# Kernel tuning notes

Measured on AMD Instinct MI355X. Metric: run time of the kernel, lower is better.

Reference implementation:

```python
import jax, jax.numpy as jnp
import numpy as np

H = 768    # bert hidden size
P = 64     # num dialogue pairs
L = 2 * P  # interleaved (user,system) sequence length
C = 2      # num_classes (CRF tags)
LAM = 0.1  # lambda_mle


def setup_inputs():
    key = jax.random.key(0)
    ks = jax.random.split(key, 21)
    def rn(k, shape, s=0.05):
        return jax.random.normal(k, shape, dtype=jnp.float32) * s
    G = 4 * H
    return {
        "user_repr": rn(ks[0], (P, H), 1.0),
        "system_repr": rn(ks[1], (P, H), 1.0),
        "post_Wih0": rn(ks[2], (2, G, H)), "post_Whh0": rn(ks[3], (2, G, H)), "post_b0": rn(ks[4], (2, G)),
        "post_Wih1": rn(ks[5], (2, G, 2 * H)), "post_Whh1": rn(ks[6], (2, G, H)), "post_b1": rn(ks[7], (2, G)),
        "prior_Wih0": rn(ks[8], (2, G, H)), "prior_Whh0": rn(ks[9], (2, G, H)), "prior_b0": rn(ks[10], (2, G)),
        "prior_Wih1": rn(ks[11], (2, G, 2 * H)), "prior_Whh1": rn(ks[12], (2, G, H)), "prior_b1": rn(ks[13], (2, G)),
        "post_proj_W": rn(ks[14], (C, 2 * H)), "post_proj_b": rn(ks[15], (C,)),
        "prior_proj_W": rn(ks[16], (C, 2 * H)), "prior_proj_b": rn(ks[17], (C,)),
        "transitions": rn(ks[18], (C, C), 0.1),
        "user_I_label": jax.random.randint(ks[19], (1, P), 0, C),
        "system_I_label": jax.random.randint(ks[20], (1, P), 0, C),
    }


def _lstm_dir(x, mask, Wih, Whh, b, reverse):
    # x: [P, L, Din]; mask: [P, L] bool (True = valid step). Masked steps freeze state,
    # so each row computes the LSTM over its own prefix exactly as the per-pair loop does.
    Pn, Ln, _ = x.shape
    Hn = Whh.shape[1]
    xw = jnp.einsum('pld,gd->plg', x, Wih) + b  # [P, L, 4H] input projections (torch gate order i,f,g,o)
    def step(carry, inp):
        h, c = carry
        xw_t, m_t = inp
        gates = xw_t + h @ Whh.T
        i, f, g, o = jnp.split(gates, 4, axis=-1)
        c2 = jax.nn.sigmoid(f) * c + jax.nn.sigmoid(i) * jnp.tanh(g)
        h2 = jax.nn.sigmoid(o) * jnp.tanh(c2)
        m = m_t[:, None]
        h = jnp.where(m, h2, h)
        c = jnp.where(m, c2, c)
        return (h, c), h
    init = (jnp.zeros((Pn, Hn), x.dtype), jnp.zeros((Pn, Hn), x.dtype))
    _, hs = jax.lax.scan(step, init, (jnp.swapaxes(xw, 0, 1), mask.T), reverse=reverse)
    return jnp.swapaxes(hs, 0, 1)  # [P, L, H]


def _bilstm(x, mask, layers):
    for Wih, Whh, b in layers:
        fwd = _lstm_dir(x, mask, Wih[0], Whh[0], b[0], False)
        bwd = _lstm_dir(x, mask, Wih[1], Whh[1], b[1], True)
        x = jnp.concatenate([fwd, bwd], axis=-1)
    return x


def _forward(user_repr, system_repr,
             post_Wih0, post_Whh0, post_b0, post_Wih1, post_Whh1, post_b1,
             prior_Wih0, prior_Whh0, prior_b0, prior_Wih1, prior_Whh1, prior_b1,
             post_proj_W, post_proj_b, prior_proj_W, prior_proj_b, transitions, labs):
    seq = jnp.stack([user_repr, system_repr], axis=1).reshape(L, H)  # interleaved u0,s0,u1,s1,...
    l = 2 * (jnp.arange(P) + 1)                 # prefix length per pair
    t = jnp.arange(L)
    mask = t[None, :] < l[:, None]              # [P, L]
    xb = jnp.broadcast_to(seq[None], (P, L, H))
    # posterior branch: biLSTM over each prefix, then emissions
    post_out = _bilstm(xb, mask, [(post_Wih0, post_Whh0, post_b0), (post_Wih1, post_Whh1, post_b1)])
    em = post_out @ post_proj_W.T + post_proj_b  # [P, L, C]
    mf = mask.astype(em.dtype)
    # CRF gold score per pair
    e_lab = jnp.take_along_axis(em, jnp.broadcast_to(labs[None, :, None], (P, L, 1)), axis=2)[..., 0]
    trans_step = transitions[labs[:-1], labs[1:]]  # [L-1]
    gold = (e_lab * mf).sum(1) + (trans_step[None, :] * mf[:, 1:]).sum(1)
    # CRF forward algorithm (log partition), masked scan over time
    def fstep(alpha, inp):
        em_t, m_t = inp  # [P, C], [P]
        new = jax.nn.logsumexp(alpha[:, :, None] + transitions[None, :, :] + em_t[:, None, :], axis=1)
        return jnp.where(m_t[:, None], new, alpha), None
    alpha, _ = jax.lax.scan(fstep, em[:, 0, :], (jnp.swapaxes(em[:, 1:, :], 0, 1), mask[:, 1:].T))
    total = jax.nn.logsumexp(alpha, axis=1)
    loss_crf = jnp.mean(total - gold)
    # prior branch: prefix minus last token, take last valid hidden
    mask_p = t[None, :] < (l - 1)[:, None]
    prior_out = _bilstm(xb, mask_p, [(prior_Wih0, prior_Whh0, prior_b0), (prior_Wih1, prior_Whh1, prior_b1)])
    prior_last = jnp.take_along_axis(prior_out, jnp.broadcast_to((l - 2)[:, None, None], (P, 1, 2 * H)), axis=1)[:, 0, :]
    prior_emis = prior_last @ prior_proj_W.T + prior_proj_b  # [P, C]
    post_last = jnp.take_along_axis(em, jnp.broadcast_to((l - 1)[:, None, None], (P, 1, C)), axis=1)[:, 0, :]
    loss_mle = jnp.mean((prior_emis - jax.lax.stop_gradient(post_last)) ** 2)
    return loss_crf, loss_mle, loss_crf + LAM * loss_mle


def reference(user_repr, system_repr,
              post_Wih0, post_Whh0, post_b0, post_Wih1, post_Whh1, post_b1,
              prior_Wih0, prior_Whh0, prior_b0, prior_Wih1, prior_Whh1, prior_b1,
              post_proj_W, post_proj_b, prior_proj_W, prior_proj_b, transitions,
              user_I_label, system_I_label):
    labs = jnp.stack([user_I_label[0], system_I_label[0]], axis=1).reshape(L)
    return _forward(user_repr, system_repr,
                    post_Wih0, post_Whh0, post_b0, post_Wih1, post_Whh1, post_b1,
                    prior_Wih0, prior_Whh0, prior_b0, prior_Wih1, prior_Whh1, prior_b1,
                    post_proj_W, post_proj_b, prior_proj_W, prior_proj_b, transitions, labs)
```

## Files before the change

kernel.cpp:

```cpp
#include <hip/hip_runtime.h>


typedef short v8s __attribute__((ext_vector_type(8)));
typedef float v4f __attribute__((ext_vector_type(4)));
typedef unsigned short u16;

#define MFMA(a, b, c) __builtin_amdgcn_mfma_f32_16x16x32_bf16((a), (b), (c), 0, 0, 0)

static constexpr size_t WMAT    = (size_t)96 * 3072 * 8;
static constexpr size_t SLOT64  = (size_t)96 * 64 * 8;
static constexpr size_t SLOT16  = (size_t)96 * 16 * 8;
static constexpr size_t SLOT128 = (size_t)96 * 128 * 8;

static constexpr size_t OFF_CALL = 0;
static constexpr size_t SZ_CALL  = (size_t)8 * 64 * 768 * 4;
static constexpr size_t OFF_EM   = OFF_CALL + SZ_CALL;
static constexpr size_t SZ_EM    = (size_t)2 * 64 * 128 * 2 * 4;
static constexpr size_t OFF_XW0  = OFF_EM + SZ_EM;
static constexpr size_t SZ_XW    = (size_t)4 * 128 * 3072 * 4;
static constexpr size_t OFF_XW1  = OFF_XW0 + SZ_XW;
static constexpr size_t OFF_SEQ  = OFF_XW1 + SZ_XW;
static constexpr size_t SZ_SEQ   = (size_t)96 * 128 * 8 * 2;
static constexpr size_t OFF_LABS = OFF_SEQ + SZ_SEQ;
static constexpr size_t SZ_LABS  = 512;
static constexpr size_t OFF_W0   = OFF_LABS + SZ_LABS;
static constexpr size_t SZ_W4    = (size_t)4 * WMAT * 2;
static constexpr size_t OFF_W1X  = OFF_W0 + SZ_W4;
static constexpr size_t OFF_W1R  = OFF_W1X + SZ_W4;
static constexpr size_t OFF_F0   = OFF_W1R + SZ_W4;
static constexpr size_t SZ_F0    = (size_t)2 * 129 * SLOT16 * 2;
static constexpr size_t OFF_H0F  = OFF_F0 + SZ_F0;
static constexpr size_t SZ_H0F   = (size_t)2 * SLOT128 * 2;
static constexpr size_t OFF_B0   = OFF_H0F + SZ_H0F;
static constexpr size_t SZ_S64   = (size_t)2 * 129 * SLOT64 * 2;
static constexpr size_t OFF_F1   = OFF_B0 + SZ_S64;
static constexpr size_t OFF_B1   = OFF_F1 + SZ_S64;
static constexpr size_t WS_NEED  = OFF_B1 + SZ_S64;

static __device__ __forceinline__ u16 f2b(float f) {
  unsigned int u = __float_as_uint(f);
  unsigned int r = (u + 0x7FFFu + ((u >> 16) & 1u)) >> 16;
  return (u16)r;
}
static __device__ __forceinline__ float b2f(u16 u) {
  return __uint_as_float(((unsigned int)u) << 16);
}
static __device__ __forceinline__ float sigf(float x) {
  return 1.0f / (1.0f + __expf(-x));
}
static __device__ __forceinline__ float tanhfast(float x) {
  return 1.0f - 2.0f / (__expf(2.0f * x) + 1.0f);
}
static __device__ __forceinline__ float lse2(float a, float b) {
  float mx = fmaxf(a, b);
  return mx + __logf(__expf(a - mx) + __expf(b - mx));
}

static __device__ __forceinline__ void stage_w(const u16* mat, int kb0, int jb, u16* lds) {
  const int4* src = (const int4*)mat;
  int4* dst = (int4*)lds;
  int tid = threadIdx.x;
#pragma unroll
  for (int it = 0; it < 12; ++it) {
    int ck = it * 256 + tid;
    int kb = ck >> 6;
    int r = ck & 63;
    int g = (r >> 4) * 768 + jb + (r & 15);
    dst[ck] = src[(size_t)(kb0 + kb) * 3072 + g];
  }
}

__global__ void init_zero(float* c_all, u16* f0a, u16* f0b, u16* b0a, u16* b0b,
                          u16* f1a, u16* f1b, u16* b1a, u16* b1b) {
  int idx = blockIdx.x * 256 + threadIdx.x;
  c_all[idx] = 0.0f;
  if (idx < (int)SLOT16) { f0a[idx] = 0; f0b[idx] = 0; }
  if (idx < (int)SLOT64) {
    b0a[idx] = 0; b0b[idx] = 0;
    f1a[idx] = 0; f1b[idx] = 0;
    b1a[idx] = 0; b1b[idx] = 0;
  }
}

__global__ void build_seq(const float* user, const float* sysr, const int* ulab,
                          const int* slab, u16* seqkp, int* labs) {
  int idx = blockIdx.x * 256 + threadIdx.x;
  int t = idx / 768;
  int hh = idx - t * 768;
  float v = (t & 1) ? sysr[(t >> 1) * 768 + hh] : user[(t >> 1) * 768 + hh];
  seqkp[((size_t)(hh >> 3) * 128 + t) * 8 + (hh & 7)] = f2b(v);
  if (idx < 128) labs[idx] = (idx & 1) ? slab[idx >> 1] : ulab[idx >> 1];
}

__global__ void cvt_w(const float* postWhh0, const float* priWhh0,
                      const float* postWih1, const float* priWih1,
                      const float* postWhh1, const float* priWhh1,
                      u16* W0kp, u16* W1xkp, u16* W1rkp) {
  int mat = blockIdx.y;
  int grp = mat >> 2;
  int sub = mat & 3;
  int m = sub >> 1;
  int dirw = sub & 1;
  const float* src;
  int stride, coff;
  u16* dstb;
  if (grp == 0)      { src = m ? priWhh0 : postWhh0; stride = 768;  coff = 0;   dstb = W0kp; }
  else if (grp == 1) { src = m ? priWih1 : postWih1; stride = 1536; coff = 768; dstb = W1xkp; }
  else               { src = m ? priWhh1 : postWhh1; stride = 768;  coff = 0;   dstb = W1rkp; }
  src += (size_t)dirw * 3072 * stride;
  int cid = blockIdx.x * 256 + threadIdx.x;
  int g = cid / 96;
  int kb = cid - g * 96;
  const float* s = src + (size_t)g * stride + coff + (size_t)kb * 8;
  union { u16 h[8]; int4 v; } u;
#pragma unroll
  for (int j = 0; j < 8; ++j) u.h[j] = f2b(s[j]);
  ((int4*)(dstb + (size_t)sub * WMAT))[(size_t)kb * 3072 + g] = u.v;
}

__global__ void __launch_bounds__(256) xw_gemm(const u16* Akp, unsigned long long Astride,
                                               const float* Wm0, const float* Wm1, int wstride,
                                               const float* bm0, const float* bm1, float* out) {
  __shared__ u16 lds[48 * 64 * 8];
  int tid = threadIdx.x;
  int lane = tid & 63;
  int wave = tid >> 6;
  int md = blockIdx.y;
  int m = md >> 1;
  int dir = md & 1;
  const u16* A = Akp + (size_t)m * Astride;
  const float* W = (m ? Wm1 : Wm0) + (size_t)dir * 3072 * wstride;
  const float* b = (m ? bm1 : bm0) + dir * 3072;
  int g0 = blockIdx.x * 64;
  int quad = lane >> 4, l15 = lane & 15;
  v4f acc[2][4];
#pragma unroll
  for (int a = 0; a < 2; ++a)
#pragma unroll
    for (int nt = 0; nt < 4; ++nt) acc[a][nt] = (v4f){0.f, 0.f, 0.f, 0.f};

  for (int hfl = 0; hfl < 2; ++hfl) {
    if (hfl) __syncthreads();
    for (int it = 0; it < 12; ++it) {
      int ck = it * 256 + tid;
      int kb = ck >> 6;
      int r = ck & 63;
      int g = g0 + r;
      const float* s = W + (size_t)g * wstride + (size_t)(hfl * 48 + kb) * 8;
      union { u16 h[8]; int4 v; } u;
#pragma unroll
      for (int j = 0; j < 8; ++j) u.h[j] = f2b(s[j]);
      *(int4*)(lds + (size_t)ck * 8) = u.v;
    }
    __syncthreads();
    for (int lt = 0; lt < 12; ++lt) {
      int kblk = (hfl * 12 + lt) * 4 + quad;
      v8s a0 = ((const v8s*)A)[(size_t)kblk * 128 + (wave * 2 + 0) * 16 + l15];
      v8s a1 = ((const v8s*)A)[(size_t)kblk * 128 + (wave * 2 + 1) * 16 + l15];
#pragma unroll
      for (int nt = 0; nt < 4; ++nt) {
        v8s bb = *(const v8s*)(lds + ((size_t)((lt * 4 + quad) * 64) + nt * 16 + l15) * 8);
        acc[0][nt] = MFMA(a0, bb, acc[0][nt]);
        acc[1][nt] = MFMA(a1, bb, acc[1][nt]);
      }
    }
  }
#pragma unroll
  for (int a = 0; a < 2; ++a)
#pragma unroll
    for (int nt = 0; nt < 4; ++nt) {
      int g = g0 + nt * 16 + l15;
      float bv = b[g];
#pragma unroll
      for (int r = 0; r < 4; ++r) {
        int trow = (wave * 2 + a) * 16 + quad * 4 + r;
        out[(size_t)(md * 128 + trow) * 3072 + g] = acc[a][nt][r] + bv;
      }
    }
}

__global__ void __launch_bounds__(256) stepA_k(int t, const u16* W0kp, const float* xw0,
                                               u16* B0, u16* F0, u16* h0f, float* c_all) {
  __shared__ u16 lds[48 * 64 * 8];
  int tid = threadIdx.x;
  int lane = tid & 63;
  int wave = tid >> 6;
  int c = blockIdx.y;
  int isf = c >> 1;
  int m = c & 1;
  int dir = isf ? 0 : 1;
  int jb = blockIdx.x * 16;
  int quad = lane >> 4, l15 = lane & 15;
  const u16* mat = W0kp + (size_t)(m * 2 + dir) * WMAT;
  const u16* Asrc;
  int R, rowbase;
  if (isf) { Asrc = F0 + (size_t)(m * 129 + t) * SLOT16; R = 16; rowbase = 0; }
  else     { Asrc = B0 + (size_t)(m * 129 + t + 1) * SLOT64; R = 64; rowbase = wave * 16; }
  v4f acc[4];
#pragma unroll
  for (int gt = 0; gt < 4; ++gt) acc[gt] = (v4f){0.f, 0.f, 0.f, 0.f};
  bool docomp = (!isf) || (wave == 0);

  for (int hfl = 0; hfl < 2; ++hfl) {
    if (hfl) __syncthreads();
    stage_w(mat, hfl * 48, jb, lds);
    __syncthreads();
    if (docomp) {
      for (int lt = 0; lt < 12; ++lt) {
        int kblk = hfl * 48 + lt * 4 + quad;
        v8s a = ((const v8s*)Asrc)[(size_t)kblk * R + rowbase + l15];
#pragma unroll
        for (int gt = 0; gt < 4; ++gt) {
          v8s bb = *(const v8s*)(lds + ((size_t)((lt * 4 + quad) * 4 + gt) * 16 + l15) * 8);
          acc[gt] = MFMA(a, bb, acc[gt]);
        }
      }
    }
  }
  if (!docomp) return;

  int j = jb + l15;
  const float* xw = xw0 + (size_t)((m * 2 + dir) * 128 + t) * 3072;
  float xi = xw[j], xf = xw[768 + j], xg = xw[1536 + j], xo = xw[2304 + j];
  float* cs = c_all + (size_t)c * 64 * 768;
  if (!isf) {
    u16* dst = B0 + (size_t)(m * 129 + t) * SLOT64;
#pragma unroll
    for (int r = 0; r < 4; ++r) {
      int p = wave * 16 + quad * 4 + r;
      float gi = sigf(acc[0][r] + xi), gf = sigf(acc[1][r] + xf);
      float gg = tanhfast(acc[2][r] + xg), go = sigf(acc[3][r] + xo);
      float cold = cs[(size_t)p * 768 + j];
      float cn = gf * cold + gi * gg;
      float hn = go * tanhfast(cn);
      int lenp = 2 * p + 2 - m;
      bool act = t < lenp;
      float ce = act ? cn : 0.f;
      float he = act ? hn : 0.f;
      cs[(size_t)p * 768 + j] = ce;
      dst[((size_t)(j >> 3) * 64 + p) * 8 + (j & 7)] = f2b(he);
    }
  } else {
    if (quad == 0) {
      float gi = sigf(acc[0][0] + xi), gf = sigf(acc[1][0] + xf);
      float gg = tanhfast(acc[2][0] + xg), go = sigf(acc[3][0] + xo);
      float cold = cs[j];
      float cn = gf * cold + gi * gg;
      float hn = go * tanhfast(cn);
      cs[j] = cn;
      F0[(size_t)(m * 129 + t + 1) * SLOT16 + ((size_t)(j >> 3) * 16) * 8 + (j & 7)] = f2b(hn);
      h0f[(size_t)m * SLOT128 + ((size_t)(j >> 3) * 128 + t) * 8 + (j & 7)] = f2b(hn);
    }
  }
}

__global__ void __launch_bounds__(256) stepB_k(int t, const u16* W1x, const u16* W1r,
                                               const float* xw1s, const u16* B0, u16* F1,
                                               u16* B1, float* c_all) {
  __shared__ u16 lds[48 * 64 * 8];
  int tid = threadIdx.x;
  int lane = tid & 63;
  int wave = tid >> 6;
  int md = blockIdx.y;
  int m = md >> 1;
  int dir = md & 1;
  int jb = blockIdx.x * 16;
  int quad = lane >> 4, l15 = lane & 15;
  const u16* A1 = B0 + (size_t)(m * 129 + t) * SLOT64;
  const u16* A2 = dir ? (const u16*)(B1 + (size_t)(m * 129 + t + 1) * SLOT64)
                      : (const u16*)(F1 + (size_t)(m * 129 + t) * SLOT64);
  v4f acc[4];
#pragma unroll
  for (int gt = 0; gt < 4; ++gt) acc[gt] = (v4f){0.f, 0.f, 0.f, 0.f};

  for (int q = 0; q < 4; ++q) {
    if (q) __syncthreads();
    const u16* mat = (q < 2 ? W1x : W1r) + (size_t)md * WMAT;
    stage_w(mat, (q & 1) * 48, jb, lds);
    __syncthreads();
    const u16* As = (q < 2) ? A1 : A2;
    int akb0 = (q & 1) * 48;
    for (int lt = 0; lt < 12; ++lt) {
      v8s a = ((const v8s*)As)[(size_t)(akb0 + lt * 4 + quad) * 64 + wave * 16 + l15];
#pragma unroll
      for (int gt = 0; gt < 4; ++gt) {
        v8s bb = *(const v8s*)(lds + ((size_t)((lt * 4 + quad) * 4 + gt) * 16 + l15) * 8);
        acc[gt] = MFMA(a, bb, acc[gt]);
      }
    }
  }

  int j = jb + l15;
  const float* xw = xw1s + (size_t)(md * 128 + t) * 3072;
  float xi = xw[j], xf = xw[768 + j], xg = xw[1536 + j], xo = xw[2304 + j];
  float* cs = c_all + (size_t)(4 + md) * 64 * 768;
  u16* dst = dir ? (B1 + (size_t)(m * 129 + t) * SLOT64)
                 : (F1 + (size_t)(m * 129 + t + 1) * SLOT64);
  const u16* F1t = F1 + (size_t)(m * 129 + t) * SLOT64;
#pragma unroll
  for (int r = 0; r < 4; ++r) {
    int p = wave * 16 + quad * 4 + r;
    float gi = sigf(acc[0][r] + xi), gf = sigf(acc[1][r] + xf);
    float gg = tanhfast(acc[2][r] + xg), go = sigf(acc[3][r] + xo);
    float cold = cs[(size_t)p * 768 + j];
    float cn = gf * cold + gi * gg;
    float hn = go * tanhfast(cn);
    int lenp = 2 * p + 2 - m;
    bool act = t < lenp;
    float he, ce;
    if (!dir) {
      if (act) { he = hn; ce = cn; }
      else { he = b2f(F1t[((size_t)(j >> 3) * 64 + p) * 8 + (j & 7)]); ce = cold; }
    } else {
      he = act ? hn : 0.f;
      ce = act ? cn : 0.f;
    }
    cs[(size_t)p * 768 + j] = ce;
    dst[((size_t)(j >> 3) * 64 + p) * 8 + (j & 7)] = f2b(he);
  }
}

__global__ void __launch_bounds__(256) em_k(const u16* F1, const u16* B1,
                                            const float* pW0, const float* pb0,
                                            const float* pW1, const float* pb1, float* em) {
  int wid = blockIdx.x * 4 + (threadIdx.x >> 6);
  int lane = threadIdx.x & 63;
  int m = wid >> 13;
  int rem = wid & 8191;
  int p = rem >> 7;
  int t = rem & 127;
  const u16* hf = F1 + (size_t)(m * 129 + t + 1) * SLOT64;
  const u16* hb = B1 + (size_t)(m * 129 + t) * SLOT64;
  const float* Pw = m ? pW1 : pW0;
  const float* Pb = m ? pb1 : pb0;
  float s0 = 0.f, s1 = 0.f;
#pragma unroll
  for (int i = 0; i < 12; ++i) {
    int j = i * 64 + lane;
    size_t o = ((size_t)(j >> 3) * 64 + p) * 8 + (j & 7);
    float vf = b2f(hf[o]);
    float vb = b2f(hb[o]);
    s0 += Pw[j] * vf + Pw[768 + j] * vb;
    s1 += Pw[1536 + j] * vf + Pw[2304 + j] * vb;
  }
  for (int off = 32; off; off >>= 1) {
    s0 += __shfl_down(s0, off, 64);
    s1 += __shfl_down(s1, off, 64);
  }
  if (lane == 0) {
    em[((size_t)(m * 64 + p) * 128 + t) * 2 + 0] = s0 + Pb[0];
    em[((size_t)(m * 64 + p) * 128 + t) * 2 + 1] = s1 + Pb[1];
  }
}

__global__ void final_k(const float* em, const int* labs, const float* T, float* out) {
  int p = threadIdx.x;
  const float* emP = em + (size_t)p * 128 * 2;
  int lp = 2 * p + 2;
  float T00 = T[0], T01 = T[1], T10 = T[2], T11 = T[3];
  int prevlab = labs[0];
  float gold = emP[prevlab];
  for (int t = 1; t < lp; ++t) {
    int lb = labs[t];
    gold += emP[t * 2 + lb] + (prevlab ? (lb ? T11 : T10) : (lb ? T01 : T00));
    prevlab = lb;
  }
  float a0 = emP[0], a1 = emP[1];
  for (int t = 1; t < lp; ++t) {
    float n0 = lse2(a0 + T00, a1 + T10) + emP[t * 2];
    float n1 = lse2(a0 + T01, a1 + T11) + emP[t * 2 + 1];
    a0 = n0;
    a1 = n1;
  }
  float crf = lse2(a0, a1) - gold;
  const float* emR = em + (size_t)(64 + p) * 128 * 2;
  int lpr = 2 * p + 1;
  float d0 = emR[(lpr - 1) * 2 + 0] - emP[(lp - 1) * 2 + 0];
  float d1 = emR[(lpr - 1) * 2 + 1] - emP[(lp - 1) * 2 + 1];
  float mse = d0 * d0 + d1 * d1;
  for (int off = 32; off; off >>= 1) {
    crf += __shfl_down(crf, off, 64);
    mse += __shfl_down(mse, off, 64);
  }
  if (p == 0) {
    float lc = crf / 64.f;
    float lm = mse / 128.f;
    out[0] = lc;
    out[1] = lm;
    out[2] = lc + 0.1f * lm;
  }
}

extern "C" void kernel_launch(void* const* d_in, const int* in_sizes, int n_in,
                              void* d_out, int out_size, void* d_ws, size_t ws_size,
                              hipStream_t stream) {
  (void)in_sizes; (void)n_in; (void)out_size;
  if (ws_size < WS_NEED) return;

  const float* user     = (const float*)d_in[0];
  const float* sysr     = (const float*)d_in[1];
  const float* postWih0 = (const float*)d_in[2];
  const float* postWhh0 = (const float*)d_in[3];
  const float* postb0   = (const float*)d_in[4];
  const float* postWih1 = (const float*)d_in[5];
  const float* postWhh1 = (const float*)d_in[6];
  const float* postb1   = (const float*)d_in[7];
  const float* priWih0  = (const float*)d_in[8];
  const float* priWhh0  = (const float*)d_in[9];
  const float* prib0    = (const float*)d_in[10];
  const float* priWih1  = (const float*)d_in[11];
  const float* priWhh1  = (const float*)d_in[12];
  const float* prib1    = (const float*)d_in[13];
  const float* postPW   = (const float*)d_in[14];
  const float* postPb   = (const float*)d_in[15];
  const float* priPW    = (const float*)d_in[16];
  const float* priPb    = (const float*)d_in[17];
  const float* trans    = (const float*)d_in[18];
  const int*   ulab     = (const int*)d_in[19];
  const int*   slab     = (const int*)d_in[20];
  float* out = (float*)d_out;

  char* w = (char*)d_ws;
  float* c_all = (float*)(w + OFF_CALL);
  float* em    = (float*)(w + OFF_EM);
  float* xw0   = (float*)(w + OFF_XW0);
  float* xw1s  = (float*)(w + OFF_XW1);
  u16* seqkp   = (u16*)(w + OFF_SEQ);
  int* labs    = (int*)(w + OFF_LABS);
  u16* W0kp    = (u16*)(w + OFF_W0);
  u16* W1xkp   = (u16*)(w + OFF_W1X);
  u16* W1rkp   = (u16*)(w + OFF_W1R);
  u16* F0      = (u16*)(w + OFF_F0);
  u16* h0f     = (u16*)(w + OFF_H0F);
  u16* B0      = (u16*)(w + OFF_B0);
  u16* F1      = (u16*)(w + OFF_F1);
  u16* B1      = (u16*)(w + OFF_B1);

  init_zero<<<1536, 256, 0, stream>>>(
      c_all,
      F0, F0 + (size_t)129 * SLOT16,
      B0 + (size_t)128 * SLOT64, B0 + (size_t)(129 + 128) * SLOT64,
      F1, F1 + (size_t)129 * SLOT64,
      B1 + (size_t)128 * SLOT64, B1 + (size_t)(129 + 128) * SLOT64);

  build_seq<<<384, 256, 0, stream>>>(user, sysr, ulab, slab, seqkp, labs);

  cvt_w<<<dim3(1152, 12), 256, 0, stream>>>(postWhh0, priWhh0, postWih1, priWih1,
                                            postWhh1, priWhh1, W0kp, W1xkp, W1rkp);

  xw_gemm<<<dim3(48, 4), 256, 0, stream>>>(seqkp, 0ULL, postWih0, priWih0, 768,
                                           postb0, prib0, xw0);

  for (int t = 0; t < 128; ++t)
    stepA_k<<<dim3(48, 4), 256, 0, stream>>>(t, W0kp, xw0, B0, F0, h0f, c_all);

  xw_gemm<<<dim3(48, 4), 256, 0, stream>>>(h0f, (unsigned long long)SLOT128,
                                           postWih1, priWih1, 1536, postb1, prib1, xw1s);

  for (int t = 0; t < 128; ++t)
    stepB_k<<<dim3(48, 4), 256, 0, stream>>>(t, W1xkp, W1rkp, xw1s, B0, F1, B1, c_all);

  em_k<<<4096, 256, 0, stream>>>(F1, B1, postPW, postPb, priPW, priPb, em);

  final_k<<<1, 64, 0, stream>>>(em, labs, trans, out);
}
```

Baseline: 4.053 ms.

## Replace per-step LSTM kernel launches with persistent kernels using grid barriers

The 256 per-timestep launches for the two LSTM layers become two persistent kernels of 192 blocks. Each block keeps its slice of the recurrent weights resident in LDS, loaded via global_load_lds, and cell state in registers. Steps are synchronised with per-chain atomic grid barriers. The weights are repacked so all four gates of a unit sit together, and phase 2 double-buffers streaming of the input weights. This removes launch overhead and repeated weight staging, but relies on all 192 blocks being co-resident and on a spin barrier that has a timeout guard.

```diff
diff --git a/kernel.cpp b/kernel.cpp
--- a/kernel.cpp
+++ b/kernel.cpp
@@ -8,22 +8,20 @@
 #define MFMA(a, b, c) __builtin_amdgcn_mfma_f32_16x16x32_bf16((a), (b), (c), 0, 0, 0)
 
 static constexpr size_t WMAT    = (size_t)96 * 3072 * 8;
+static constexpr size_t SLOT16  = (size_t)96 * 16 * 8;
 static constexpr size_t SLOT64  = (size_t)96 * 64 * 8;
-static constexpr size_t SLOT16  = (size_t)96 * 16 * 8;
 static constexpr size_t SLOT128 = (size_t)96 * 128 * 8;
 
-static constexpr size_t OFF_CALL = 0;
-static constexpr size_t SZ_CALL  = (size_t)8 * 64 * 768 * 4;
-static constexpr size_t OFF_EM   = OFF_CALL + SZ_CALL;
+static constexpr size_t OFF_EM   = 0;
 static constexpr size_t SZ_EM    = (size_t)2 * 64 * 128 * 2 * 4;
 static constexpr size_t OFF_XW0  = OFF_EM + SZ_EM;
 static constexpr size_t SZ_XW    = (size_t)4 * 128 * 3072 * 4;
 static constexpr size_t OFF_XW1  = OFF_XW0 + SZ_XW;
 static constexpr size_t OFF_SEQ  = OFF_XW1 + SZ_XW;
-static constexpr size_t SZ_SEQ   = (size_t)96 * 128 * 8 * 2;
+static constexpr size_t SZ_SEQ   = SLOT128 * 2;
 static constexpr size_t OFF_LABS = OFF_SEQ + SZ_SEQ;
-static constexpr size_t SZ_LABS  = 512;
-static constexpr size_t OFF_W0   = OFF_LABS + SZ_LABS;
+static constexpr size_t OFF_BAR  = OFF_LABS + 512;
+static constexpr size_t OFF_W0   = OFF_BAR + 1024;
 static constexpr size_t SZ_W4    = (size_t)4 * WMAT * 2;
 static constexpr size_t OFF_W1X  = OFF_W0 + SZ_W4;
 static constexpr size_t OFF_W1R  = OFF_W1X + SZ_W4;
@@ -56,30 +54,39 @@
   return mx + __logf(__expf(a - mx) + __expf(b - mx));
 }
 
-static __device__ __forceinline__ void stage_w(const u16* mat, int kb0, int jb, u16* lds) {
-  const int4* src = (const int4*)mat;
-  int4* dst = (int4*)lds;
-  int tid = threadIdx.x;
-#pragma unroll
-  for (int it = 0; it < 12; ++it) {
-    int ck = it * 256 + tid;
-    int kb = ck >> 6;
-    int r = ck & 63;
-    int g = (r >> 4) * 768 + jb + (r & 15);
-    dst[ck] = src[(size_t)(kb0 + kb) * 3072 + g];
-  }
-}
-
-__global__ void init_zero(float* c_all, u16* f0a, u16* f0b, u16* b0a, u16* b0b,
-                          u16* f1a, u16* f1b, u16* b1a, u16* b1b) {
+static __device__ __forceinline__ void gl2lds16(const void* g, void* l) {
+  __builtin_amdgcn_global_load_lds((const __attribute__((address_space(1))) unsigned int*)g,
+                                   (__attribute__((address_space(3))) unsigned int*)l,
+                                   16, 0, 0);
+}
+
+static __device__ __forceinline__ void bar_nosync(unsigned* bar, unsigned nblk) {
+  if (threadIdx.x == 0) {
+    unsigned gen = __hip_atomic_load(bar + 1, __ATOMIC_RELAXED, __HIP_MEMORY_SCOPE_AGENT);
+    unsigned got = __hip_atomic_fetch_add(bar, 1u, __ATOMIC_ACQ_REL, __HIP_MEMORY_SCOPE_AGENT);
+    if (got == nblk - 1u) {
+      __hip_atomic_store(bar, 0u, __ATOMIC_RELAXED, __HIP_MEMORY_SCOPE_AGENT);
+      __hip_atomic_fetch_add(bar + 1, 1u, __ATOMIC_RELEASE, __HIP_MEMORY_SCOPE_AGENT);
+    } else {
+      int guard = 0;
+      while (__hip_atomic_load(bar + 1, __ATOMIC_RELAXED, __HIP_MEMORY_SCOPE_AGENT) == gen) {
+        __builtin_amdgcn_s_sleep(2);
+        if (++guard > (1 << 20)) break;
+      }
+      __threadfence();
+    }
+  }
+  __syncthreads();
+}
+
+__global__ void init_zero(u16* f0a, u16* f0b, u16* b0a, u16* b0b,
+                          u16* f1a, u16* f1b, u16* b1a, u16* b1b, unsigned* bars) {
   int idx = blockIdx.x * 256 + threadIdx.x;
-  c_all[idx] = 0.0f;
   if (idx < (int)SLOT16) { f0a[idx] = 0; f0b[idx] = 0; }
-  if (idx < (int)SLOT64) {
-    b0a[idx] = 0; b0b[idx] = 0;
-    f1a[idx] = 0; f1b[idx] = 0;
-    b1a[idx] = 0; b1b[idx] = 0;
-  }
+  b0a[idx] = 0; b0b[idx] = 0;
+  f1a[idx] = 0; f1b[idx] = 0;
+  b1a[idx] = 0; b1b[idx] = 0;
+  if (idx < 256) bars[idx] = 0;
 }
 
 __global__ void build_seq(const float* user, const float* sysr, const int* ulab,
@@ -99,23 +106,26 @@
   int mat = blockIdx.y;
   int grp = mat >> 2;
   int sub = mat & 3;
-  int m = sub >> 1;
+  int mm = sub >> 1;
   int dirw = sub & 1;
   const float* src;
   int stride, coff;
   u16* dstb;
-  if (grp == 0)      { src = m ? priWhh0 : postWhh0; stride = 768;  coff = 0;   dstb = W0kp; }
-  else if (grp == 1) { src = m ? priWih1 : postWih1; stride = 1536; coff = 768; dstb = W1xkp; }
-  else               { src = m ? priWhh1 : postWhh1; stride = 768;  coff = 0;   dstb = W1rkp; }
+  if (grp == 0)      { src = mm ? priWhh0 : postWhh0; stride = 768;  coff = 0;   dstb = W0kp; }
+  else if (grp == 1) { src = mm ? priWih1 : postWih1; stride = 1536; coff = 768; dstb = W1xkp; }
+  else               { src = mm ? priWhh1 : postWhh1; stride = 768;  coff = 0;   dstb = W1rkp; }
   src += (size_t)dirw * 3072 * stride;
   int cid = blockIdx.x * 256 + threadIdx.x;
   int g = cid / 96;
   int kb = cid - g * 96;
+  int gate = g / 768;
+  int unit = g - gate * 768;
+  int gp = unit * 4 + gate;
   const float* s = src + (size_t)g * stride + coff + (size_t)kb * 8;
   union { u16 h[8]; int4 v; } u;
 #pragma unroll
   for (int j = 0; j < 8; ++j) u.h[j] = f2b(s[j]);
-  ((int4*)(dstb + (size_t)sub * WMAT))[(size_t)kb * 3072 + g] = u.v;
+  ((int4*)(dstb + (size_t)sub * WMAT))[(size_t)kb * 3072 + gp] = u.v;
 }
 
 __global__ void __launch_bounds__(256) xw_gemm(const u16* Akp, unsigned long long Astride,
@@ -179,144 +189,232 @@
     }
 }
 
-__global__ void __launch_bounds__(256) stepA_k(int t, const u16* W0kp, const float* xw0,
-                                               u16* B0, u16* F0, u16* h0f, float* c_all) {
-  __shared__ u16 lds[48 * 64 * 8];
-  int tid = threadIdx.x;
-  int lane = tid & 63;
-  int wave = tid >> 6;
-  int c = blockIdx.y;
-  int isf = c >> 1;
-  int m = c & 1;
-  int dir = isf ? 0 : 1;
-  int jb = blockIdx.x * 16;
-  int quad = lane >> 4, l15 = lane & 15;
-  const u16* mat = W0kp + (size_t)(m * 2 + dir) * WMAT;
-  const u16* Asrc;
-  int R, rowbase;
-  if (isf) { Asrc = F0 + (size_t)(m * 129 + t) * SLOT16; R = 16; rowbase = 0; }
-  else     { Asrc = B0 + (size_t)(m * 129 + t + 1) * SLOT64; R = 64; rowbase = wave * 16; }
-  v4f acc[4];
-#pragma unroll
-  for (int gt = 0; gt < 4; ++gt) acc[gt] = (v4f){0.f, 0.f, 0.f, 0.f};
-  bool docomp = (!isf) || (wave == 0);
-
-  for (int hfl = 0; hfl < 2; ++hfl) {
-    if (hfl) __syncthreads();
-    stage_w(mat, hfl * 48, jb, lds);
+__global__ void __launch_bounds__(256, 1) phase1_k(const u16* W0kp, const float* xw0,
+                                                   u16* B0, u16* F0, u16* h0f,
+                                                   unsigned* bars) {
+  extern __shared__ u16 ldsraw[];
+  v8s* lw = (v8s*)ldsraw;
+  const int tid = threadIdx.x;
+  const int w = tid >> 6, lane = tid & 63, l15 = lane & 15, l4 = lane >> 4;
+  const int b = blockIdx.x;
+  const int chain = (b & 7) >> 1;
+  const int ci = ((b >> 3) << 1) | (b & 1);
+  const int jb = ci << 4;
+  const int m = chain & 1;
+  const bool isf = chain >= 2;
+  const int mat = m * 2 + (isf ? 0 : 1);
+  unsigned* bar = bars + chain * 32;
+
+  {
+    const v8s* Ws = (const v8s*)(W0kp) + (size_t)mat * (WMAT / 8);
+    const size_t rowb = (size_t)jb * 4;
+    for (int i = 0; i < 24; ++i) {
+      int idx = i * 256 + tid;
+      int kg = idx >> 6, r = idx & 63;
+      gl2lds16(Ws + (size_t)kg * 3072 + rowb + r, (void*)(lw + (i * 256 + (w << 6))));
+    }
+  }
+  __syncthreads();
+
+  const int i0 = w >> 1, j0 = w & 1;
+  const int u0 = i0 * 8 + l4, u1 = u0 + 4;
+  const int ju0 = jb + u0, ju1 = jb + u1;
+  const int p0q = j0 * 32 + l15, p1q = p0q + 16;
+  float c00 = 0.f, c01 = 0.f, c10 = 0.f, c11 = 0.f;
+  const bool skip = isf && (j0 == 1);
+  const bool fep  = isf && (j0 == 0) && (l15 == 0);
+
+  for (int it = 0; it < 128; ++it) {
+    const int t = isf ? it : (127 - it);
+    const float* xw = xw0 + (size_t)(mat * 128 + t) * 3072;
+    float xi0 = xw[ju0], xf0 = xw[768 + ju0], xg0 = xw[1536 + ju0], xo0 = xw[2304 + ju0];
+    float xi1 = xw[ju1], xf1 = xw[768 + ju1], xg1 = xw[1536 + ju1], xo1 = xw[2304 + ju1];
+    v4f a00 = {0.f, 0.f, 0.f, 0.f}, a01 = a00, a10 = a00, a11 = a00;
+
+    if (isf) {
+      if (!skip) {
+        const v8s* hs = (const v8s*)(F0 + (size_t)(m * 129 + t) * SLOT16);
+#pragma unroll
+        for (int kb = 0; kb < 24; ++kb) {
+          int kg = kb * 4 + l4;
+          v8s A0 = lw[kg * 64 + i0 * 32 + l15];
+          v8s A1 = lw[kg * 64 + i0 * 32 + 16 + l15];
+          v8s Bb = hs[kg * 16 + l15];
+          a00 = MFMA(A0, Bb, a00);
+          a10 = MFMA(A1, Bb, a10);
+        }
+      }
+    } else {
+      const v8s* hs = (const v8s*)(B0 + (size_t)(m * 129 + t + 1) * SLOT64);
+#pragma unroll
+      for (int kb = 0; kb < 24; ++kb) {
+        int kg = kb * 4 + l4;
+        v8s A0 = lw[kg * 64 + i0 * 32 + l15];
+        v8s A1 = lw[kg * 64 + i0 * 32 + 16 + l15];
+        v8s Bb0 = hs[kg * 64 + p0q];
+        v8s Bb1 = hs[kg * 64 + p1q];
+        a00 = MFMA(A0, Bb0, a00);
+        a01 = MFMA(A0, Bb1, a01);
+        a10 = MFMA(A1, Bb0, a10);
+        a11 = MFMA(A1, Bb1, a11);
+      }
+    }
+
+    if (isf) {
+      if (fep) {
+        float gi = sigf(a00[0] + xi0), gf = sigf(a00[1] + xf0);
+        float gg = tanhfast(a00[2] + xg0), go = sigf(a00[3] + xo0);
+        float cn = gf * c00 + gi * gg;
+        float hn = go * tanhfast(cn);
+        c00 = cn;
+        u16 hb = f2b(hn);
+        F0[(size_t)(m * 129 + t + 1) * SLOT16 + (size_t)(ju0 >> 3) * 16 * 8 + (ju0 & 7)] = hb;
+        h0f[(size_t)m * SLOT128 + ((size_t)(ju0 >> 3) * 128 + t) * 8 + (ju0 & 7)] = hb;
+        gi = sigf(a10[0] + xi1); gf = sigf(a10[1] + xf1);
+        gg = tanhfast(a10[2] + xg1); go = sigf(a10[3] + xo1);
+        cn = gf * c10 + gi * gg;
+        hn = go * tanhfast(cn);
+        c10 = cn;
+        hb = f2b(hn);
+        F0[(size_t)(m * 129 + t + 1) * SLOT16 + (size_t)(ju1 >> 3) * 16 * 8 + (ju1 & 7)] = hb;
+        h0f[(size_t)m * SLOT128 + ((size_t)(ju1 >> 3) * 128 + t) * 8 + (ju1 & 7)] = hb;
+      }
+    } else {
+      u16* hd = B0 + (size_t)(m * 129 + t) * SLOT64;
+      auto epi1 = [&](const v4f& ac, float& cc, int ju, int p,
+                      float xi, float xf, float xg, float xo) {
+        int lenp = 2 * p + 2 - m;
+        bool act = t < lenp;
+        float gi = sigf(ac[0] + xi), gf = sigf(ac[1] + xf);
+        float gg = tanhfast(ac[2] + xg), go = sigf(ac[3] + xo);
+        float cn = gf * cc + gi * gg;
+        float hn = go * tanhfast(cn);
+        cc = act ? cn : 0.f;
+        hd[((size_t)(ju >> 3) * 64 + p) * 8 + (ju & 7)] = f2b(act ? hn : 0.f);
+      };
+      epi1(a00, c00, ju0, p0q, xi0, xf0, xg0, xo0);
+      epi1(a01, c01, ju0, p1q, xi0, xf0, xg0, xo0);
+      epi1(a10, c10, ju1, p0q, xi1, xf1, xg1, xo1);
+      epi1(a11, c11, ju1, p1q, xi1, xf1, xg1, xo1);
+    }
+    __threadfence();
     __syncthreads();
-    if (docomp) {
-      for (int lt = 0; lt < 12; ++lt) {
-        int kblk = hfl * 48 + lt * 4 + quad;
-        v8s a = ((const v8s*)Asrc)[(size_t)kblk * R + rowbase + l15];
-#pragma unroll
-        for (int gt = 0; gt < 4; ++gt) {
-          v8s bb = *(const v8s*)(lds + ((size_t)((lt * 4 + quad) * 4 + gt) * 16 + l15) * 8);
-          acc[gt] = MFMA(a, bb, acc[gt]);
-        }
-      }
-    }
-  }
-  if (!docomp) return;
-
-  int j = jb + l15;
-  const float* xw = xw0 + (size_t)((m * 2 + dir) * 128 + t) * 3072;
-  float xi = xw[j], xf = xw[768 + j], xg = xw[1536 + j], xo = xw[2304 + j];
-  float* cs = c_all + (size_t)c * 64 * 768;
-  if (!isf) {
-    u16* dst = B0 + (size_t)(m * 129 + t) * SLOT64;
-#pragma unroll
-    for (int r = 0; r < 4; ++r) {
-      int p = wave * 16 + quad * 4 + r;
-      float gi = sigf(acc[0][r] + xi), gf = sigf(acc[1][r] + xf);
-      float gg = tanhfast(acc[2][r] + xg), go = sigf(acc[3][r] + xo);
-      float cold = cs[(size_t)p * 768 + j];
-      float cn = gf * cold + gi * gg;
-      float hn = go * tanhfast(cn);
+    bar_nosync(bar, 48u);
+  }
+}
+
+__global__ void __launch_bounds__(256, 1) phase2_k(const u16* W1x, const u16* W1r,
+                                                   const float* xw1s, const u16* B0,
+                                                   u16* F1, u16* B1, unsigned* bars) {
+  extern __shared__ u16 ldsraw[];
+  v8s* lwr = (v8s*)ldsraw;
+  u16* bufb = ldsraw + 49152;
+  const int tid = threadIdx.x;
+  const int w = tid >> 6, lane = tid & 63, l15 = lane & 15, l4 = lane >> 4;
+  const int b = blockIdx.x;
+  const int md = (b & 7) >> 1;
+  const int ci = ((b >> 3) << 1) | (b & 1);
+  const int jb = ci << 4;
+  const int m = md >> 1, dir = md & 1;
+  unsigned* bar = bars + (4 + md) * 32;
+  const size_t rowb = (size_t)jb * 4;
+  const v8s* Wxs = (const v8s*)(W1x) + (size_t)md * (WMAT / 8);
+
+  {
+    const v8s* Wrs = (const v8s*)(W1r) + (size_t)md * (WMAT / 8);
+    for (int i = 0; i < 24; ++i) {
+      int idx = i * 256 + tid;
+      int kg = idx >> 6, r = idx & 63;
+      gl2lds16(Wrs + (size_t)kg * 3072 + rowb + r, (void*)(lwr + (i * 256 + (w << 6))));
+    }
+  }
+
+  const int i0 = w >> 1, j0 = w & 1;
+  const int u0 = i0 * 8 + l4, u1 = u0 + 4;
+  const int ju0 = jb + u0, ju1 = jb + u1;
+  const int p0q = j0 * 32 + l15, p1q = p0q + 16;
+  float c00 = 0.f, c01 = 0.f, c10 = 0.f, c11 = 0.f;
+  float he00 = 0.f, he01 = 0.f, he10 = 0.f, he11 = 0.f;
+
+  auto stage = [&](int c, int v) {
+#pragma unroll
+    for (int q = 0; q < 6; ++q) {
+      int idx = q * 256 + tid;
+      int kgl = idx >> 6, r = idx & 63;
+      gl2lds16(Wxs + (size_t)(c * 24 + kgl) * 3072 + rowb + r,
+               (void*)(bufb + (size_t)v * 12288 + (size_t)(q * 256 + (w << 6)) * 8));
+    }
+  };
+  stage(0, 0);
+  __syncthreads();
+
+  for (int it = 0; it < 128; ++it) {
+    const int t = dir ? (127 - it) : it;
+    const v8s* hx = (const v8s*)(B0 + (size_t)(m * 129 + t) * SLOT64);
+    const v8s* hr = (const v8s*)(dir ? (B1 + (size_t)(m * 129 + t + 1) * SLOT64)
+                                     : (F1 + (size_t)(m * 129 + t) * SLOT64));
+    const float* xw = xw1s + (size_t)(md * 128 + t) * 3072;
+    float xi0 = xw[ju0], xf0 = xw[768 + ju0], xg0 = xw[1536 + ju0], xo0 = xw[2304 + ju0];
+    float xi1 = xw[ju1], xf1 = xw[768 + ju1], xg1 = xw[1536 + ju1], xo1 = xw[2304 + ju1];
+    v4f a00 = {0.f, 0.f, 0.f, 0.f}, a01 = a00, a10 = a00, a11 = a00;
+
+    auto rpart = [&](int k0) {
+#pragma unroll
+      for (int k = 0; k < 8; ++k) {
+        int kg = (k0 + k) * 4 + l4;
+        v8s A0 = lwr[kg * 64 + i0 * 32 + l15];
+        v8s A1 = lwr[kg * 64 + i0 * 32 + 16 + l15];
+        v8s Bb0 = hr[kg * 64 + p0q];
+        v8s Bb1 = hr[kg * 64 + p1q];
+        a00 = MFMA(A0, Bb0, a00); a01 = MFMA(A0, Bb1, a01);
+        a10 = MFMA(A1, Bb0, a10); a11 = MFMA(A1, Bb1, a11);
+      }
+    };
+    auto xpart = [&](int c, int v) {
+      const v8s* bv = (const v8s*)(bufb + (size_t)v * 12288);
+#pragma unroll
+      for (int k = 0; k < 6; ++k) {
+        int kgl = k * 4 + l4;
+        int kg = (c * 6 + k) * 4 + l4;
+        v8s A0 = bv[kgl * 64 + i0 * 32 + l15];
+        v8s A1 = bv[kgl * 64 + i0 * 32 + 16 + l15];
+        v8s Bb0 = hx[kg * 64 + p0q];
+        v8s Bb1 = hx[kg * 64 + p1q];
+        a00 = MFMA(A0, Bb0, a00); a01 = MFMA(A0, Bb1, a01);
+        a10 = MFMA(A1, Bb0, a10); a11 = MFMA(A1, Bb1, a11);
+      }
+    };
+
+    stage(1, 1); rpart(0);  xpart(0, 0); __syncthreads();
+    stage(2, 0); rpart(8);  xpart(1, 1); __syncthreads();
+    stage(3, 1); rpart(16); xpart(2, 0); __syncthreads();
+    xpart(3, 1);
+
+    u16* hd = dir ? (B1 + (size_t)(m * 129 + t) * SLOT64)
+                  : (F1 + (size_t)(m * 129 + t + 1) * SLOT64);
+    auto epi = [&](const v4f& ac, float& cc, float& he, int ju, int p,
+                   float xi, float xf, float xg, float xo) {
       int lenp = 2 * p + 2 - m;
       bool act = t < lenp;
-      float ce = act ? cn : 0.f;
-      float he = act ? hn : 0.f;
-      cs[(size_t)p * 768 + j] = ce;
-      dst[((size_t)(j >> 3) * 64 + p) * 8 + (j & 7)] = f2b(he);
-    }
-  } else {
-    if (quad == 0) {
-      float gi = sigf(acc[0][0] + xi), gf = sigf(acc[1][0] + xf);
-      float gg = tanhfast(acc[2][0] + xg), go = sigf(acc[3][0] + xo);
-      float cold = cs[j];
-      float cn = gf * cold + gi * gg;
+      float gi = sigf(ac[0] + xi), gf = sigf(ac[1] + xf);
+      float gg = tanhfast(ac[2] + xg), go = sigf(ac[3] + xo);
+      float cn = gf * cc + gi * gg;
       float hn = go * tanhfast(cn);
-      cs[j] = cn;
-      F0[(size_t)(m * 129 + t + 1) * SLOT16 + ((size_t)(j >> 3) * 16) * 8 + (j & 7)] = f2b(hn);
-      h0f[(size_t)m * SLOT128 + ((size_t)(j >> 3) * 128 + t) * 8 + (j & 7)] = f2b(hn);
-    }
-  }
-}
-
-__global__ void __launch_bounds__(256) stepB_k(int t, const u16* W1x, const u16* W1r,
-                                               const float* xw1s, const u16* B0, u16* F1,
-                                               u16* B1, float* c_all) {
-  __shared__ u16 lds[48 * 64 * 8];
-  int tid = threadIdx.x;
-  int lane = tid & 63;
-  int wave = tid >> 6;
-  int md = blockIdx.y;
-  int m = md >> 1;
-  int dir = md & 1;
-  int jb = blockIdx.x * 16;
-  int quad = lane >> 4, l15 = lane & 15;
-  const u16* A1 = B0 + (size_t)(m * 129 + t) * SLOT64;
-  const u16* A2 = dir ? (const u16*)(B1 + (size_t)(m * 129 + t + 1) * SLOT64)
-                      : (const u16*)(F1 + (size_t)(m * 129 + t) * SLOT64);
-  v4f acc[4];
-#pragma unroll
-  for (int gt = 0; gt < 4; ++gt) acc[gt] = (v4f){0.f, 0.f, 0.f, 0.f};
-
-  for (int q = 0; q < 4; ++q) {
-    if (q) __syncthreads();
-    const u16* mat = (q < 2 ? W1x : W1r) + (size_t)md * WMAT;
-    stage_w(mat, (q & 1) * 48, jb, lds);
+      float hv;
+      if (dir) { hv = act ? hn : 0.f;  cc = act ? cn : 0.f; }
+      else     { hv = act ? hn : he;   cc = act ? cn : cc;  }
+      he = hv;
+      hd[((size_t)(ju >> 3) * 64 + p) * 8 + (ju & 7)] = f2b(hv);
+    };
+    epi(a00, c00, he00, ju0, p0q, xi0, xf0, xg0, xo0);
+    epi(a01, c01, he01, ju0, p1q, xi0, xf0, xg0, xo0);
+    epi(a10, c10, he10, ju1, p0q, xi1, xf1, xg1, xo1);
+    epi(a11, c11, he11, ju1, p1q, xi1, xf1, xg1, xo1);
+
+    __threadfence();
     __syncthreads();
-    const u16* As = (q < 2) ? A1 : A2;
-    int akb0 = (q & 1) * 48;
-    for (int lt = 0; lt < 12; ++lt) {
-      v8s a = ((const v8s*)As)[(size_t)(akb0 + lt * 4 + quad) * 64 + wave * 16 + l15];
-#pragma unroll
-      for (int gt = 0; gt < 4; ++gt) {
-        v8s bb = *(const v8s*)(lds + ((size_t)((lt * 4 + quad) * 4 + gt) * 16 + l15) * 8);
-        acc[gt] = MFMA(a, bb, acc[gt]);
-      }
-    }
-  }
-
-  int j = jb + l15;
-  const float* xw = xw1s + (size_t)(md * 128 + t) * 3072;
-  float xi = xw[j], xf = xw[768 + j], xg = xw[1536 + j], xo = xw[2304 + j];
-  float* cs = c_all + (size_t)(4 + md) * 64 * 768;
-  u16* dst = dir ? (B1 + (size_t)(m * 129 + t) * SLOT64)
-                 : (F1 + (size_t)(m * 129 + t + 1) * SLOT64);
-  const u16* F1t = F1 + (size_t)(m * 129 + t) * SLOT64;
-#pragma unroll
-  for (int r = 0; r < 4; ++r) {
-    int p = wave * 16 + quad * 4 + r;
-    float gi = sigf(acc[0][r] + xi), gf = sigf(acc[1][r] + xf);
-    float gg = tanhfast(acc[2][r] + xg), go = sigf(acc[3][r] + xo);
-    float cold = cs[(size_t)p * 768 + j];
-    float cn = gf * cold + gi * gg;
-    float hn = go * tanhfast(cn);
-    int lenp = 2 * p + 2 - m;
-    bool act = t < lenp;
-    float he, ce;
-    if (!dir) {
-      if (act) { he = hn; ce = cn; }
-      else { he = b2f(F1t[((size_t)(j >> 3) * 64 + p) * 8 + (j & 7)]); ce = cold; }
-    } else {
-      he = act ? hn : 0.f;
-      ce = act ? cn : 0.f;
-    }
-    cs[(size_t)p * 768 + j] = ce;
-    dst[((size_t)(j >> 3) * 64 + p) * 8 + (j & 7)] = f2b(he);
+    stage(0, 0);
+    bar_nosync(bar, 48u);
   }
 }
 
@@ -420,28 +518,36 @@
   const int*   slab     = (const int*)d_in[20];
   float* out = (float*)d_out;
 
-  char* w = (char*)d_ws;
-  float* c_all = (float*)(w + OFF_CALL);
-  float* em    = (float*)(w + OFF_EM);
-  float* xw0   = (float*)(w + OFF_XW0);
-  float* xw1s  = (float*)(w + OFF_XW1);
-  u16* seqkp   = (u16*)(w + OFF_SEQ);
-  int* labs    = (int*)(w + OFF_LABS);
-  u16* W0kp    = (u16*)(w + OFF_W0);
-  u16* W1xkp   = (u16*)(w + OFF_W1X);
-  u16* W1rkp   = (u16*)(w + OFF_W1R);
-  u16* F0      = (u16*)(w + OFF_F0);
-  u16* h0f     = (u16*)(w + OFF_H0F);
-  u16* B0      = (u16*)(w + OFF_B0);
-  u16* F1      = (u16*)(w + OFF_F1);
-  u16* B1      = (u16*)(w + OFF_B1);
-
-  init_zero<<<1536, 256, 0, stream>>>(
-      c_all,
+  char* wsb = (char*)d_ws;
+  float* em    = (float*)(wsb + OFF_EM);
+  float* xw0   = (float*)(wsb + OFF_XW0);
+  float* xw1s  = (float*)(wsb + OFF_XW1);
+  u16* seqkp   = (u16*)(wsb + OFF_SEQ);
+  int* labs    = (int*)(wsb + OFF_LABS);
+  unsigned* bars = (unsigned*)(wsb + OFF_BAR);
+  u16* W0kp    = (u16*)(wsb + OFF_W0);
+  u16* W1xkp   = (u16*)(wsb + OFF_W1X);
+  u16* W1rkp   = (u16*)(wsb + OFF_W1R);
+  u16* F0      = (u16*)(wsb + OFF_F0);
+  u16* h0f     = (u16*)(wsb + OFF_H0F);
+  u16* B0      = (u16*)(wsb + OFF_B0);
+  u16* F1      = (u16*)(wsb + OFF_F1);
+  u16* B1      = (u16*)(wsb + OFF_B1);
+
+  static bool attr_done = false;
+  if (!attr_done) {
+    (void)hipFuncSetAttribute(reinterpret_cast<const void*>(phase1_k),
+                              hipFuncAttributeMaxDynamicSharedMemorySize, 98304);
+    (void)hipFuncSetAttribute(reinterpret_cast<const void*>(phase2_k),
+                              hipFuncAttributeMaxDynamicSharedMemorySize, 147456);
+    attr_done = true;
+  }
+
+  init_zero<<<192, 256, 0, stream>>>(
       F0, F0 + (size_t)129 * SLOT16,
       B0 + (size_t)128 * SLOT64, B0 + (size_t)(129 + 128) * SLOT64,
       F1, F1 + (size_t)129 * SLOT64,
-      B1 + (size_t)128 * SLOT64, B1 + (size_t)(129 + 128) * SLOT64);
+      B1 + (size_t)128 * SLOT64, B1 + (size_t)(129 + 128) * SLOT64, bars);
 
   build_seq<<<384, 256, 0, stream>>>(user, sysr, ulab, slab, seqkp, labs);
 
@@ -451,14 +557,12 @@
   xw_gemm<<<dim3(48, 4), 256, 0, stream>>>(seqkp, 0ULL, postWih0, priWih0, 768,
                                            postb0, prib0, xw0);
 
-  for (int t = 0; t < 128; ++t)
-    stepA_k<<<dim3(48, 4), 256, 0, stream>>>(t, W0kp, xw0, B0, F0, h0f, c_all);
+  phase1_k<<<192, 256, 98304, stream>>>(W0kp, xw0, B0, F0, h0f, bars);
 
   xw_gemm<<<dim3(48, 4), 256, 0, stream>>>(h0f, (unsigned long long)SLOT128,
                                            postWih1, priWih1, 1536, postb1, prib1, xw1s);
 
-  for (int t = 0; t < 128; ++t)
-    stepB_k<<<dim3(48, 4), 256, 0, stream>>>(t, W1xkp, W1rkp, xw1s, B0, F1, B1, c_all);
+  phase2_k<<<192, 256, 147456, stream>>>(W1xkp, W1rkp, xw1s, B0, F1, B1, bars);
 
   em_k<<<4096, 256, 0, stream>>>(F1, B1, postPW, postPb, priPW, priPb, em);
 
```

Result: slower. 8.596 ms (+112.1%).
